# Kernel tuning notes

Measured on AMD Instinct MI355X. Metric: run time of the kernel, lower is better.

## Reference

```python
import jax, jax.numpy as jnp
import numpy as np

HIDDEN = 3584
NUM_HEADS = 28
NUM_KV_HEADS = 4
HEAD_DIM = 128
ROPE_THETA = 1000000.0
B, S = 2, 2048


def setup_inputs() -> dict:
    key = jax.random.key(0)
    k1, k2, k3, k4 = jax.random.split(key, 4)
    q_size = NUM_HEADS * HEAD_DIM
    kv_size = NUM_KV_HEADS * HEAD_DIM
    return {
        "positions": jnp.arange(B * S, dtype=jnp.int32).reshape(B, S),
        "hidden_states": jax.random.normal(k1, (B, S, HIDDEN), dtype=jnp.float32),
        "w_qkv": jax.random.normal(k2, (HIDDEN, q_size + 2 * kv_size), dtype=jnp.float32) * (HIDDEN ** -0.5),
        "b_qkv": jax.random.normal(k3, (q_size + 2 * kv_size,), dtype=jnp.float32) * 0.02,
        "w_o": jax.random.normal(k4, (q_size, HIDDEN), dtype=jnp.float32) * (q_size ** -0.5),
    }


def _rope_cos_sin(positions):
    # NeoX-style rotary embedding, rotary_dim == head_dim
    half = HEAD_DIM // 2
    inv_freq = 1.0 / (ROPE_THETA ** (jnp.arange(0, half, dtype=jnp.float32) * 2.0 / HEAD_DIM))
    angles = positions.astype(jnp.float32)[..., None] * inv_freq  # [B, S, half]
    return jnp.cos(angles), jnp.sin(angles)


def _apply_rope(x, cos, sin):
    # x: [B, S, H, D]; cos/sin: [B, S, half] -> broadcast over heads
    x1, x2 = jnp.split(x, 2, axis=-1)
    c = cos[:, :, None, :]
    s = sin[:, :, None, :]
    return jnp.concatenate([x1 * c - x2 * s, x2 * c + x1 * s], axis=-1)


def reference(positions, hidden_states, w_qkv, b_qkv, w_o):
    q_size = NUM_HEADS * HEAD_DIM
    kv_size = NUM_KV_HEADS * HEAD_DIM
    scaling = HEAD_DIM ** -0.5
    groups = NUM_HEADS // NUM_KV_HEADS

    qkv = hidden_states @ w_qkv + b_qkv  # [B, S, q+2kv]
    q, k, v = jnp.split(qkv, [q_size, q_size + kv_size], axis=-1)
    q = q.reshape(B, S, NUM_HEADS, HEAD_DIM)
    k = k.reshape(B, S, NUM_KV_HEADS, HEAD_DIM)
    v = v.reshape(B, S, NUM_KV_HEADS, HEAD_DIM)

    cos, sin = _rope_cos_sin(positions)
    q = _apply_rope(q, cos, sin)
    k = _apply_rope(k, cos, sin)

    # GQA: group query heads over kv heads. q: [B, S, Hkv, G, D]
    qg = q.reshape(B, S, NUM_KV_HEADS, groups, HEAD_DIM)
    scores = jnp.einsum("bqhgd,bkhd->bhgqk", qg, k) * scaling  # [B, Hkv, G, S, S]
    causal = jnp.tril(jnp.ones((S, S), dtype=bool))
    scores = jnp.where(causal, scores, jnp.finfo(scores.dtype).min)
    probs = jax.nn.softmax(scores, axis=-1)
    o = jnp.einsum("bhgqk,bkhd->bqhgd", probs, v)  # [B, S, Hkv, G, D]
    o = o.reshape(B, S, NUM_HEADS * HEAD_DIM)
    return o @ w_o  # [B, S, HIDDEN]
```

## Files before the change

### kernel.cpp

```cpp
#include <hip/hip_runtime.h>

typedef unsigned short u16;
typedef unsigned int u32;
typedef __bf16 bf16x8 __attribute__((ext_vector_type(8)));
typedef float f32x4 __attribute__((ext_vector_type(4)));

#define NHEAD 28
#define NKVH 4
#define HD 128
#define NB 2
#define NS 2048
#define NTOK 4096
#define HIDDEN_DIM 3584
#define QKVW 4608
#define QSZ 3584
#define KOFF 3584
#define VOFF 4096
#define VSLAB (NTOK * 512)
#define NJOBS 896
#define ATTN_BLOCKS 512
#define QSCALE_L2E 0.12751744f

__device__ __forceinline__ float bf2f(u16 u) {
  u32 x = ((u32)u) << 16; float f; __builtin_memcpy(&f, &x, 4); return f;
}
__device__ __forceinline__ u16 f2bf(float f) {
  u32 x; __builtin_memcpy(&x, &f, 4);
  x += 0x7FFFu + ((x >> 16) & 1u);
  return (u16)(x >> 16);
}
__device__ __forceinline__ u32 pack2bf(float a, float b) {
  __bf16 lo = (__bf16)a, hi = (__bf16)b;
  u16 ul, uh;
  __builtin_memcpy(&ul, &lo, 2); __builtin_memcpy(&uh, &hi, 2);
  return (u32)ul | ((u32)uh << 16);
}
__device__ __forceinline__ void async16(const void* g, void* lds) {
  __builtin_amdgcn_global_load_lds((const __attribute__((address_space(1))) void*)g,
                                   (__attribute__((address_space(3))) void*)lds,
                                   16, 0, 0);
}

#define SB __builtin_amdgcn_sched_barrier(0)
#define BAR do { SB; __builtin_amdgcn_s_barrier(); SB; } while (0)

__global__ void cast_f32_bf16(const float* __restrict__ in, u16* __restrict__ out) {
  int i = (blockIdx.x * 256 + threadIdx.x) * 4;
  float4 v = *(const float4*)(in + i);
  u32 p0 = (u32)f2bf(v.x) | ((u32)f2bf(v.y) << 16);
  u32 p1 = (u32)f2bf(v.z) | ((u32)f2bf(v.w) << 16);
  uint2 r; r.x = p0; r.y = p1;
  *(uint2*)(out + i) = r;
}

__global__ void transpose_cast(const float* __restrict__ in, u16* __restrict__ out,
                               int R, int C) {
  __shared__ float tile[32][33];
  int tx = threadIdx.x & 31, ty = threadIdx.x >> 5;
  int c0 = blockIdx.x * 32, r0 = blockIdx.y * 32;
#pragma unroll
  for (int i = 0; i < 32; i += 8)
    tile[ty + i][tx] = in[(size_t)(r0 + ty + i) * C + c0 + tx];
  __syncthreads();
#pragma unroll
  for (int i = 0; i < 32; i += 8)
    out[(size_t)(c0 + ty + i) * R + r0 + tx] = f2bf(tile[tx][ty + i]);
}

__global__ void rope_table(const int* __restrict__ positions,
                           float* __restrict__ cs, float* __restrict__ sn,
                           int* __restrict__ ctr) {
  if (blockIdx.x == 0 && threadIdx.x == 0) *ctr = 0;
  int idx = blockIdx.x * 256 + threadIdx.x;
  int t = idx >> 6, i = idx & 63;
  float p = (float)positions[t];
  float inv = expf(-(float)i * (13.815510557964274f / 64.f));
  float a = p * inv;
  cs[idx] = cosf(a);
  sn[idx] = sinf(a);
}

__global__ void rope_kernel(u16* __restrict__ qkv, const float* __restrict__ cs,
                            const float* __restrict__ sn) {
  int w = threadIdx.x >> 6, l = threadIdx.x & 63;
  int rid = blockIdx.x * 4 + w;
  int t = rid >> 5, hh = rid & 31;
  size_t base = (size_t)t * QKVW + (hh < NHEAD ? hh * HD : KOFF + (hh - NHEAD) * HD);
  float x1 = bf2f(qkv[base + l]), x2 = bf2f(qkv[base + l + 64]);
  float c = cs[t * 64 + l], s = sn[t * 64 + l];
  float y1 = x1 * c - x2 * s;
  float y2 = x2 * c + x1 * s;
  if (hh < NHEAD) { y1 *= QSCALE_L2E; y2 *= QSCALE_L2E; }
  qkv[base + l] = f2bf(y1);
  qkv[base + l + 64] = f2bf(y2);
}

template <int MODE>
__global__ __launch_bounds__(512, 2) void gemm256(
    const u16* __restrict__ A, const u16* __restrict__ Bt,
    const float* __restrict__ bias, u16* __restrict__ outb,
    float* __restrict__ outf, int M, int Next, int Kst, int ldc, int NT) {
  __shared__ __align__(16) u16 Al[2][256 * 64];
  __shared__ __align__(16) u16 Bl[2][256 * 64];
  const int tid = threadIdx.x;
  const int l = tid & 63, w = tid >> 6;
  const int g = l >> 4, r = l & 15;
  const int wm = w >> 2, wn = w & 3;
  const int nbx = Next >> 8;
  const int cpx = (int)gridDim.x >> 3;
  const int bid = ((int)blockIdx.x & 7) * cpx + ((int)blockIdx.x >> 3);
  int bx, by, kbase;
  float* outp = outf;
  if (MODE == 2) {
    const int tps = nbx * (M >> 8);
    const int ks = bid / tps, rem = bid % tps;
    by = rem / nbx; bx = rem % nbx;
    kbase = ks * (NT << 6);
    outp = outf + (size_t)ks * M * Next;
  } else {
    bx = bid % nbx; by = bid / nbx; kbase = 0;
  }
  const int row0 = by * 256, col0 = bx * 256;

  f32x4 acc[8][4] = {};
  bf16x8 af[4][2];
  bf16x8 bfr[2][2][2];

  auto stageU = [&](const u16* mb, int base0, char* ldsMat, int h, int t) {
#pragma unroll
    for (int q = 0; q < 2; ++q) {
      const int idx = q * 512 + tid;
      const int rho = h * 128 + (idx >> 3);
      const int sl = (idx & 7) ^ (rho & 7);
      async16(mb + (size_t)(base0 + rho) * Kst + kbase + t * 64 + sl * 8,
              ldsMat + (size_t)(t & 1) * 32768 + h * 16384 + idx * 16);
    }
  };

#define READ_A(s, rh)                                                           \
  _Pragma("unroll") for (int fr = 0; fr < 4; ++fr) {                            \
    const int row_ = (rh) * 128 + wm * 64 + fr * 16 + r;                        \
    _Pragma("unroll") for (int kk = 0; kk < 2; ++kk) {                          \
      const int sl_ = (kk * 4 + g) ^ (row_ & 7);                                \
      af[fr][kk] = *(const bf16x8*)((const char*)Al + (s) * 32768 +             \
                                    row_ * 128 + sl_ * 16);                     \
    }                                                                           \
  }
#define READ_B(s, ch)                                                           \
  _Pragma("unroll") for (int fc = 0; fc < 2; ++fc) {                            \
    const int col_ = (ch) * 128 + wn * 32 + fc * 16 + r;                        \
    _Pragma("unroll") for (int kk = 0; kk < 2; ++kk) {                          \
      const int sl_ = (kk * 4 + g) ^ (col_ & 7);                                \
      bfr[ch][fc][kk] = *(const bf16x8*)((const char*)Bl + (s) * 32768 +        \
                                         col_ * 128 + sl_ * 16);                \
    }                                                                           \
  }
#define MFMA_Q(rh, ch)                                                          \
  __builtin_amdgcn_s_setprio(1);                                                \
  _Pragma("unroll") for (int fr = 0; fr < 4; ++fr)                              \
  _Pragma("unroll") for (int fc = 0; fc < 2; ++fc)                              \
  _Pragma("unroll") for (int kk = 0; kk < 2; ++kk)                              \
    acc[(rh) * 4 + fr][(ch) * 2 + fc] = __builtin_amdgcn_mfma_f32_16x16x32_bf16( \
        af[fr][kk], bfr[ch][fc][kk], acc[(rh) * 4 + fr][(ch) * 2 + fc], 0, 0, 0);\
  __builtin_amdgcn_s_setprio(0);

  stageU(A, row0, (char*)Al, 0, 0); stageU(A, row0, (char*)Al, 1, 0);
  stageU(Bt, col0, (char*)Bl, 0, 0); stageU(Bt, col0, (char*)Bl, 1, 0);
  stageU(A, row0, (char*)Al, 0, 1); stageU(Bt, col0, (char*)Bl, 0, 1);
  SB; asm volatile("s_waitcnt vmcnt(4)" ::: "memory");
  BAR;

  for (int t = 0; t < NT; ++t) {
    const int s = t & 1;
    READ_A(s, 0); READ_B(s, 0);
    if (t + 1 < NT) stageU(A, row0, (char*)Al, 1, t + 1);
    BAR; MFMA_Q(0, 0); BAR;
    READ_B(s, 1);
    if (t + 1 < NT) stageU(Bt, col0, (char*)Bl, 1, t + 1);
    BAR; MFMA_Q(0, 1); BAR;
    READ_A(s, 1);
    if (t + 2 < NT) stageU(A, row0, (char*)Al, 0, t + 2);
    BAR; MFMA_Q(1, 0); BAR;
    if (t + 2 < NT) stageU(Bt, col0, (char*)Bl, 0, t + 2);
    BAR; MFMA_Q(1, 1);
    if (t < NT - 2)        { SB; asm volatile("s_waitcnt vmcnt(4)" ::: "memory"); }
    else if (t == NT - 2)  { SB; asm volatile("s_waitcnt vmcnt(0)" ::: "memory"); }
    BAR;
  }
  SB; asm volatile("s_waitcnt vmcnt(0)" ::: "memory");

#pragma unroll
  for (int m = 0; m < 8; ++m) {
    const int row = row0 + (m >> 2) * 128 + wm * 64 + (m & 3) * 16 + g * 4;
#pragma unroll
    for (int n = 0; n < 4; ++n) {
      const int col = col0 + (n >> 1) * 128 + wn * 32 + (n & 1) * 16 + r;
      const float bb = (MODE == 0) ? bias[col] : 0.f;
#pragma unroll
      for (int j = 0; j < 4; ++j) {
        float v = acc[m][n][j] + bb;
        if (MODE == 0) outb[(size_t)(row + j) * ldc + col] = f2bf(v);
        else           outp[(size_t)(row + j) * ldc + col] = v;
      }
    }
  }
}

__global__ void v_reduce(const float* __restrict__ slabs, const float* __restrict__ bias,
                         u16* __restrict__ vtg) {
  __shared__ float tile[32][33];
  const int tx = threadIdx.x & 31, ty = threadIdx.x >> 5;
  const int c0 = blockIdx.x * 32;
  const int r0 = blockIdx.y * 32;
#pragma unroll
  for (int i = 0; i < 32; i += 8) {
    const size_t idx = (size_t)(r0 + ty + i) * 512 + c0 + tx;
    float s = slabs[idx] + slabs[idx + VSLAB] + slabs[idx + 2 * VSLAB] +
              slabs[idx + 3 * VSLAB];
    tile[ty + i][tx] = s + bias[VOFF + c0 + tx];
  }
  __syncthreads();
#pragma unroll
  for (int i = 0; i < 32; i += 8) {
    const int col = c0 + ty + i;
    const int row = r0 + tx;
    vtg[((size_t)((((row >> 11) * NKVH) + (col >> 7)) * HD + (col & 127))) * NS +
        (row & 2047)] = f2bf(tile[tx][ty + i]);
  }
}

__global__ __launch_bounds__(512) void attn_kernel(const u16* __restrict__ qkv,
                                                   const u16* __restrict__ vtg,
                                                   u16* __restrict__ Oh,
                                                   int* __restrict__ ctr) {
  __shared__ __align__(16) u16 Ks[2][64 * 128];
  __shared__ __align__(16) u16 Vt[2][128 * 64];
  __shared__ int s_job;
  const int tid = threadIdx.x, l = tid & 63, w = tid >> 6;
  const int g = l >> 4, r = l & 15;
  const int srcA = r + ((l & 16) << 1);
  const int srcB = srcA + 16;
  const bool hi = (l & 32) != 0;

  for (;;) {
    if (tid == 0) s_job = atomicAdd(ctr, 1);
    __syncthreads();
    const int jid = s_job;
    if (jid >= NJOBS) return;
    const int qtr = jid / 56;
    const int qt = 15 - qtr;
    const int bh = jid - qtr * 56;
    const int h = bh % NHEAD, b = bh / NHEAD;
    const int kvh = h / 7;
    const int q0 = qt * 128;

    const int qrow = q0 + w * 16 + r;
    const size_t qbase = (size_t)(b * NS + qrow) * QKVW + h * HD;
    bf16x8 qf[4];
#pragma unroll
    for (int ks = 0; ks < 4; ++ks)
      qf[ks] = *(const bf16x8*)(qkv + qbase + ks * 32 + g * 8);

    const u16* kb0 = qkv + (size_t)(b * NS) * QKVW + KOFF + kvh * HD;
    const u16* vb0 = vtg + (size_t)((b * NKVH + kvh) * HD) * NS;

    const u16* kap[2];
    const u16* vap[2];
#pragma unroll
    for (int i = 0; i < 2; ++i) {
      const int li = (w * 2 + i) * 64 + l;
      const int rr = li >> 4, c = li & 15;
      kap[i] = kb0 + (size_t)rr * QKVW + ((c ^ (rr & 7)) << 3);
      const int d = li >> 3, c2 = li & 7;
      vap[i] = vb0 + (size_t)d * NS + ((c2 ^ (d & 7)) << 3);
    }

    f32x4 oacc[8] = {};
    float mrun = -1e30f, lsum = 0.f;

    const int nkv = 2 * qt + 2;

    auto stageK = [&](u16* kdst) {
#pragma unroll
      for (int i = 0; i < 2; ++i) {
        async16(kap[i], (char*)kdst + (w * 2 + i) * 1024);
        kap[i] += 64 * QKVW;
      }
    };
    auto stageV = [&](u16* vdst) {
#pragma unroll
      for (int i = 0; i < 2; ++i) {
        async16(vap[i], (char*)vdst + (w * 2 + i) * 1024);
        vap[i] += 64;
      }
    };

    stageK(Ks[0]); stageV(Vt[0]);
    int cur = 0;

    for (int kvt = 0; kvt < nkv; ++kvt) {
      const int kv0 = kvt * 64;
      asm volatile("s_waitcnt vmcnt(2)" ::: "memory");
      __builtin_amdgcn_s_barrier();
      __builtin_amdgcn_sched_barrier(0);

      const bool haveNext = (kvt + 1 < nkv);
      if (haveNext) { stageK(Ks[cur ^ 1]); stageV(Vt[cur ^ 1]); }

      const bool active = kv0 <= q0 + w * 16 + 15;

      union { u32 wrd[4]; bf16x8 v; } pf[2];
      if (active) {
        f32x4 sacc[4] = {};
        const char* ksB = (const char*)Ks[cur];
        __builtin_amdgcn_s_setprio(1);
#pragma unroll
        for (int n = 0; n < 4; ++n) {
          const int key = n * 16 + r;
          const int sw = (key & 7) << 4;
#pragma unroll
          for (int ks = 0; ks < 4; ++ks) {
            bf16x8 kf = *(const bf16x8*)(ksB + key * 256 + ((ks * 64 + g * 16) ^ sw));
            sacc[n] = __builtin_amdgcn_mfma_f32_16x16x32_bf16(kf, qf[ks], sacc[n], 0, 0, 0);
          }
        }
        __builtin_amdgcn_s_setprio(0);
        if (kv0 + 63 > q0 + w * 16) {
#pragma unroll
          for (int n = 0; n < 4; ++n) {
            const int key_g = kv0 + n * 16 + g * 4;
#pragma unroll
            for (int j = 0; j < 4; ++j)
              if (key_g + j > qrow) sacc[n][j] = -1e30f;
          }
        }
        float mx = fmaxf(fmaxf(sacc[0][0], sacc[0][1]), fmaxf(sacc[0][2], sacc[0][3]));
#pragma unroll
        for (int n = 1; n < 4; ++n)
          mx = fmaxf(mx, fmaxf(fmaxf(sacc[n][0], sacc[n][1]), fmaxf(sacc[n][2], sacc[n][3])));
        if (!__all(mx <= mrun + 8.0f)) {
          mx = fmaxf(mx, __shfl_xor(mx, 16, 64));
          mx = fmaxf(mx, __shfl_xor(mx, 32, 64));
          const float mnew = fmaxf(mrun, mx);
          const float scale = __builtin_amdgcn_exp2f(mrun - mnew);
          mrun = mnew;
          lsum *= scale;
#pragma unroll
          for (int dt = 0; dt < 8; ++dt) oacc[dt] *= scale;
        }
#pragma unroll
        for (int n = 0; n < 4; ++n)
#pragma unroll
          for (int j = 0; j < 4; ++j) {
            float p = __builtin_amdgcn_exp2f(sacc[n][j] - mrun);
            sacc[n][j] = p;
            lsum += p;
          }

        u32 pk[4][2];
#pragma unroll
        for (int n = 0; n < 4; ++n) {
          pk[n][0] = pack2bf(sacc[n][0], sacc[n][1]);
          pk[n][1] = pack2bf(sacc[n][2], sacc[n][3]);
        }
#pragma unroll
        for (int ks2 = 0; ks2 < 2; ++ks2) {
          const int n0 = 2 * ks2, n1 = 2 * ks2 + 1;
#pragma unroll
          for (int hh2 = 0; hh2 < 2; ++hh2) {
            u32 a0 = (u32)__shfl((int)pk[n0][hh2], srcA, 64);
            u32 a1 = (u32)__shfl((int)pk[n1][hh2], srcA, 64);
            pf[ks2].wrd[hh2] = hi ? a1 : a0;
            u32 b0 = (u32)__shfl((int)pk[n0][hh2], srcB, 64);
            u32 b1 = (u32)__shfl((int)pk[n1][hh2], srcB, 64);
            pf[ks2].wrd[2 + hh2] = hi ? b1 : b0;
          }
        }
      }

      if (haveNext) asm volatile("s_waitcnt vmcnt(4)" ::: "memory");
      else          asm volatile("s_waitcnt vmcnt(0)" ::: "memory");
      __builtin_amdgcn_s_barrier();
      __builtin_amdgcn_sched_barrier(0);
      if (active) {
        const char* vtB = (const char*)Vt[cur];
        __builtin_amdgcn_s_setprio(1);
#pragma unroll
        for (int ks2 = 0; ks2 < 2; ++ks2) {
#pragma unroll
          for (int dt = 0; dt < 8; ++dt) {
            const int d = dt * 16 + r;
            bf16x8 vf = *(const bf16x8*)(vtB + d * 128 +
                                         ((ks2 * 64 + g * 16) ^ ((d & 7) << 4)));
            oacc[dt] = __builtin_amdgcn_mfma_f32_16x16x32_bf16(vf, pf[ks2].v, oacc[dt], 0, 0, 0);
          }
        }
        __builtin_amdgcn_s_setprio(0);
      }
      cur ^= 1;
    }

    float lr = lsum;
    lr += __shfl_xor(lr, 16, 64);
    lr += __shfl_xor(lr, 32, 64);
    const float inv = 1.f / lr;
    const size_t obase = (size_t)(b * NS + qrow) * QSZ + h * HD;
#pragma unroll
    for (int dt = 0; dt < 8; ++dt) {
      uint2 r2;
      r2.x = pack2bf(oacc[dt][0] * inv, oacc[dt][1] * inv);
      r2.y = pack2bf(oacc[dt][2] * inv, oacc[dt][3] * inv);
      *(uint2*)(Oh + obase + dt * 16 + 4 * g) = r2;
    }
  }
}

extern "C" void kernel_launch(void* const* d_in, const int* in_sizes, int n_in,
                              void* d_out, int out_size, void* d_ws, size_t ws_size,
                              hipStream_t stream) {
  const int* positions = (const int*)d_in[0];
  const float* hidden = (const float*)d_in[1];
  const float* w_qkv = (const float*)d_in[2];
  const float* b_qkv = (const float*)d_in[3];
  const float* w_o = (const float*)d_in[4];
  float* out = (float*)d_out;

  char* ws = (char*)d_ws;
  const size_t XB_OFF = 0;
  const size_t WQT_OFF = 29360128;
  const size_t QKV_OFF = WQT_OFF + 33030144;
  const size_t CS_OFF = QKV_OFF + 37748736;
  const size_t SN_OFF = CS_OFF + 1048576;
  const size_t CTR_OFF = SN_OFF + 1048576;
  const size_t WS_NEED = CTR_OFF + 64;
  if (ws_size < WS_NEED) return;

  u16* Xb = (u16*)(ws + XB_OFF);
  u16* WoT = (u16*)(ws + XB_OFF);
  u16* WqT = (u16*)(ws + WQT_OFF);
  u16* Oh = (u16*)(ws + WQT_OFF);
  u16* qkvb = (u16*)(ws + QKV_OFF);
  float* cs = (float*)(ws + CS_OFF);
  float* sn = (float*)(ws + SN_OFF);
  int* ctr = (int*)(ws + CTR_OFF);
  u16* vtg = (u16*)d_out;
  float* vslabs = (float*)((char*)d_out + 4194304);

  cast_f32_bf16<<<14336, 256, 0, stream>>>(hidden, Xb);
  transpose_cast<<<dim3(QKVW / 32, HIDDEN_DIM / 32), 256, 0, stream>>>(w_qkv, WqT, HIDDEN_DIM, QKVW);
  rope_table<<<(NTOK * 64) / 256, 256, 0, stream>>>(positions, cs, sn, ctr);

  gemm256<0><<<256, 512, 0, stream>>>(
      Xb, WqT, b_qkv, qkvb, nullptr, NTOK, 4096, HIDDEN_DIM, QKVW, HIDDEN_DIM / 64);

  gemm256<2><<<128, 512, 0, stream>>>(
      Xb, WqT + (size_t)VOFF * HIDDEN_DIM, nullptr, nullptr, vslabs,
      NTOK, 512, HIDDEN_DIM, 512, HIDDEN_DIM / 64 / 4);

  v_reduce<<<dim3(512 / 32, NTOK / 32), 256, 0, stream>>>(vslabs, b_qkv, vtg);

  rope_kernel<<<(NTOK * 32) / 4, 256, 0, stream>>>(qkvb, cs, sn);

  transpose_cast<<<dim3(HIDDEN_DIM / 32, QSZ / 32), 256, 0, stream>>>(w_o, WoT, QSZ, HIDDEN_DIM);

  attn_kernel<<<ATTN_BLOCKS, 512, 0, stream>>>(qkvb, vtg, Oh, ctr);

  gemm256<1><<<(HIDDEN_DIM / 256) * (NTOK / 256), 512, 0, stream>>>(
      Oh, WoT, nullptr, nullptr, out, NTOK, HIDDEN_DIM, QSZ, HIDDEN_DIM, QSZ / 64);
}
```

Before: 444.6 us.

## Use 4-wave attention blocks with two query tiles per wave and single-buffered V

Restructures the attention kernel so each of 4 waves handles 32 query rows (two 16-row MFMA tiles), reusing every K and V fragment read from LDS for two MFMAs. This halves LDS reads per MFMA and shrinks the block to 256 threads with a single V buffer, and the grid grows to 768 blocks. In exchange, V is now loaded at the start of each iteration behind a full vmcnt(0) wait instead of being double-buffered, which exposes more load latency. Register pressure also roughly doubles for the accumulators.

```diff
diff --git a/kernel.cpp b/kernel.cpp
--- a/kernel.cpp
+++ b/kernel.cpp
@@ -18,7 +18,7 @@
 #define VOFF 4096
 #define VSLAB (NTOK * 512)
 #define NJOBS 896
-#define ATTN_BLOCKS 512
+#define ATTN_BLOCKS 768
 #define QSCALE_L2E 0.12751744f
 
 __device__ __forceinline__ float bf2f(u16 u) {
@@ -229,12 +229,12 @@
   }
 }
 
-__global__ __launch_bounds__(512) void attn_kernel(const u16* __restrict__ qkv,
+__global__ __launch_bounds__(256) void attn_kernel(const u16* __restrict__ qkv,
                                                    const u16* __restrict__ vtg,
                                                    u16* __restrict__ Oh,
                                                    int* __restrict__ ctr) {
   __shared__ __align__(16) u16 Ks[2][64 * 128];
-  __shared__ __align__(16) u16 Vt[2][128 * 64];
+  __shared__ __align__(16) u16 Vt[128 * 64];
   __shared__ int s_job;
   const int tid = threadIdx.x, l = tid & 63, w = tid >> 6;
   const int g = l >> 4, r = l & 15;
@@ -254,64 +254,69 @@
     const int kvh = h / 7;
     const int q0 = qt * 128;
 
-    const int qrow = q0 + w * 16 + r;
-    const size_t qbase = (size_t)(b * NS + qrow) * QKVW + h * HD;
-    bf16x8 qf[4];
-#pragma unroll
-    for (int ks = 0; ks < 4; ++ks)
-      qf[ks] = *(const bf16x8*)(qkv + qbase + ks * 32 + g * 8);
+    const int qrow0 = q0 + w * 32 + r;
+    const int qrow1 = qrow0 + 16;
+    const size_t qb0 = (size_t)(b * NS + qrow0) * QKVW + h * HD;
+    const size_t qb1 = (size_t)(b * NS + qrow1) * QKVW + h * HD;
+    bf16x8 qf0[4], qf1[4];
+#pragma unroll
+    for (int ks = 0; ks < 4; ++ks) {
+      qf0[ks] = *(const bf16x8*)(qkv + qb0 + ks * 32 + g * 8);
+      qf1[ks] = *(const bf16x8*)(qkv + qb1 + ks * 32 + g * 8);
+    }
 
     const u16* kb0 = qkv + (size_t)(b * NS) * QKVW + KOFF + kvh * HD;
     const u16* vb0 = vtg + (size_t)((b * NKVH + kvh) * HD) * NS;
 
-    const u16* kap[2];
-    const u16* vap[2];
-#pragma unroll
-    for (int i = 0; i < 2; ++i) {
-      const int li = (w * 2 + i) * 64 + l;
+    const u16* kap[4];
+    const u16* vap[4];
+#pragma unroll
+    for (int i = 0; i < 4; ++i) {
+      const int li = (w * 4 + i) * 64 + l;
       const int rr = li >> 4, c = li & 15;
       kap[i] = kb0 + (size_t)rr * QKVW + ((c ^ (rr & 7)) << 3);
       const int d = li >> 3, c2 = li & 7;
       vap[i] = vb0 + (size_t)d * NS + ((c2 ^ (d & 7)) << 3);
     }
 
-    f32x4 oacc[8] = {};
-    float mrun = -1e30f, lsum = 0.f;
+    f32x4 oa0[8] = {}, oa1[8] = {};
+    float m0 = -1e30f, m1 = -1e30f, ls0 = 0.f, ls1 = 0.f;
 
     const int nkv = 2 * qt + 2;
 
     auto stageK = [&](u16* kdst) {
 #pragma unroll
-      for (int i = 0; i < 2; ++i) {
-        async16(kap[i], (char*)kdst + (w * 2 + i) * 1024);
+      for (int i = 0; i < 4; ++i) {
+        async16(kap[i], (char*)kdst + (w * 4 + i) * 1024);
         kap[i] += 64 * QKVW;
       }
     };
-    auto stageV = [&](u16* vdst) {
-#pragma unroll
-      for (int i = 0; i < 2; ++i) {
-        async16(vap[i], (char*)vdst + (w * 2 + i) * 1024);
+    auto stageV = [&]() {
+#pragma unroll
+      for (int i = 0; i < 4; ++i) {
+        async16(vap[i], (char*)Vt + (w * 4 + i) * 1024);
         vap[i] += 64;
       }
     };
 
-    stageK(Ks[0]); stageV(Vt[0]);
+    stageK(Ks[0]);
     int cur = 0;
 
     for (int kvt = 0; kvt < nkv; ++kvt) {
       const int kv0 = kvt * 64;
-      asm volatile("s_waitcnt vmcnt(2)" ::: "memory");
+      asm volatile("s_waitcnt vmcnt(0) lgkmcnt(0)" ::: "memory");
       __builtin_amdgcn_s_barrier();
       __builtin_amdgcn_sched_barrier(0);
 
+      stageV();
       const bool haveNext = (kvt + 1 < nkv);
-      if (haveNext) { stageK(Ks[cur ^ 1]); stageV(Vt[cur ^ 1]); }
-
-      const bool active = kv0 <= q0 + w * 16 + 15;
-
-      union { u32 wrd[4]; bf16x8 v; } pf[2];
+      if (haveNext) stageK(Ks[cur ^ 1]);
+
+      const bool active = kv0 <= q0 + w * 32 + 31;
+
+      union { u32 wrd[4]; bf16x8 v; } pf0[2], pf1[2];
       if (active) {
-        f32x4 sacc[4] = {};
+        f32x4 s0[4] = {}, s1[4] = {};
         const char* ksB = (const char*)Ks[cur];
         __builtin_amdgcn_s_setprio(1);
 #pragma unroll
@@ -321,59 +326,106 @@
 #pragma unroll
           for (int ks = 0; ks < 4; ++ks) {
             bf16x8 kf = *(const bf16x8*)(ksB + key * 256 + ((ks * 64 + g * 16) ^ sw));
-            sacc[n] = __builtin_amdgcn_mfma_f32_16x16x32_bf16(kf, qf[ks], sacc[n], 0, 0, 0);
+            s0[n] = __builtin_amdgcn_mfma_f32_16x16x32_bf16(kf, qf0[ks], s0[n], 0, 0, 0);
+            s1[n] = __builtin_amdgcn_mfma_f32_16x16x32_bf16(kf, qf1[ks], s1[n], 0, 0, 0);
           }
         }
         __builtin_amdgcn_s_setprio(0);
-        if (kv0 + 63 > q0 + w * 16) {
+        if (kv0 + 63 > q0 + w * 32) {
 #pragma unroll
           for (int n = 0; n < 4; ++n) {
             const int key_g = kv0 + n * 16 + g * 4;
 #pragma unroll
-            for (int j = 0; j < 4; ++j)
-              if (key_g + j > qrow) sacc[n][j] = -1e30f;
+            for (int j = 0; j < 4; ++j) {
+              if (key_g + j > qrow0) s0[n][j] = -1e30f;
+              if (key_g + j > qrow1) s1[n][j] = -1e30f;
+            }
           }
         }
-        float mx = fmaxf(fmaxf(sacc[0][0], sacc[0][1]), fmaxf(sacc[0][2], sacc[0][3]));
-#pragma unroll
-        for (int n = 1; n < 4; ++n)
-          mx = fmaxf(mx, fmaxf(fmaxf(sacc[n][0], sacc[n][1]), fmaxf(sacc[n][2], sacc[n][3])));
-        if (!__all(mx <= mrun + 8.0f)) {
-          mx = fmaxf(mx, __shfl_xor(mx, 16, 64));
-          mx = fmaxf(mx, __shfl_xor(mx, 32, 64));
-          const float mnew = fmaxf(mrun, mx);
-          const float scale = __builtin_amdgcn_exp2f(mrun - mnew);
-          mrun = mnew;
-          lsum *= scale;
-#pragma unroll
-          for (int dt = 0; dt < 8; ++dt) oacc[dt] *= scale;
+        {
+          float mx = fmaxf(fmaxf(s0[0][0], s0[0][1]), fmaxf(s0[0][2], s0[0][3]));
+#pragma unroll
+          for (int n = 1; n < 4; ++n)
+            mx = fmaxf(mx, fmaxf(fmaxf(s0[n][0], s0[n][1]), fmaxf(s0[n][2], s0[n][3])));
+          if (!__all(mx <= m0 + 8.0f)) {
+            mx = fmaxf(mx, __shfl_xor(mx, 16, 64));
+            mx = fmaxf(mx, __shfl_xor(mx, 32, 64));
+            const float mnew = fmaxf(m0, mx);
+            const float scale = __builtin_amdgcn_exp2f(m0 - mnew);
+            m0 = mnew;
+            ls0 *= scale;
+#pragma unroll
+            for (int dt = 0; dt < 8; ++dt) oa0[dt] *= scale;
+          }
+#pragma unroll
+          for (int n = 0; n < 4; ++n)
+#pragma unroll
+            for (int j = 0; j < 4; ++j) {
+              float p = __builtin_amdgcn_exp2f(s0[n][j] - m0);
+              s0[n][j] = p;
+              ls0 += p;
+            }
+          u32 pk[4][2];
+#pragma unroll
+          for (int n = 0; n < 4; ++n) {
+            pk[n][0] = pack2bf(s0[n][0], s0[n][1]);
+            pk[n][1] = pack2bf(s0[n][2], s0[n][3]);
+          }
+#pragma unroll
+          for (int ks2 = 0; ks2 < 2; ++ks2) {
+            const int n0 = 2 * ks2, n1 = 2 * ks2 + 1;
+#pragma unroll
+            for (int hh2 = 0; hh2 < 2; ++hh2) {
+              u32 a0 = (u32)__shfl((int)pk[n0][hh2], srcA, 64);
+              u32 a1 = (u32)__shfl((int)pk[n1][hh2], srcA, 64);
+              pf0[ks2].wrd[hh2] = hi ? a1 : a0;
+              u32 b0 = (u32)__shfl((int)pk[n0][hh2], srcB, 64);
+              u32 b1 = (u32)__shfl((int)pk[n1][hh2], srcB, 64);
+              pf0[ks2].wrd[2 + hh2] = hi ? b1 : b0;
+            }
+          }
         }
-#pragma unroll
-        for (int n = 0; n < 4; ++n)
-#pragma unroll
-          for (int j = 0; j < 4; ++j) {
-            float p = __builtin_amdgcn_exp2f(sacc[n][j] - mrun);
-            sacc[n][j] = p;
-            lsum += p;
-          }
-
-        u32 pk[4][2];
-#pragma unroll
-        for (int n = 0; n < 4; ++n) {
-          pk[n][0] = pack2bf(sacc[n][0], sacc[n][1]);
-          pk[n][1] = pack2bf(sacc[n][2], sacc[n][3]);
-        }
-#pragma unroll
-        for (int ks2 = 0; ks2 < 2; ++ks2) {
-          const int n0 = 2 * ks2, n1 = 2 * ks2 + 1;
-#pragma unroll
-          for (int hh2 = 0; hh2 < 2; ++hh2) {
-            u32 a0 = (u32)__shfl((int)pk[n0][hh2], srcA, 64);
-            u32 a1 = (u32)__shfl((int)pk[n1][hh2], srcA, 64);
-            pf[ks2].wrd[hh2] = hi ? a1 : a0;
-            u32 b0 = (u32)__shfl((int)pk[n0][hh2], srcB, 64);
-            u32 b1 = (u32)__shfl((int)pk[n1][hh2], srcB, 64);
-            pf[ks2].wrd[2 + hh2] = hi ? b1 : b0;
+        {
+          float mx = fmaxf(fmaxf(s1[0][0], s1[0][1]), fmaxf(s1[0][2], s1[0][3]));
+#pragma unroll
+          for (int n = 1; n < 4; ++n)
+            mx = fmaxf(mx, fmaxf(fmaxf(s1[n][0], s1[n][1]), fmaxf(s1[n][2], s1[n][3])));
+          if (!__all(mx <= m1 + 8.0f)) {
+            mx = fmaxf(mx, __shfl_xor(mx, 16, 64));
+            mx = fmaxf(mx, __shfl_xor(mx, 32, 64));
+            const float mnew = fmaxf(m1, mx);
+            const float scale = __builtin_amdgcn_exp2f(m1 - mnew);
+            m1 = mnew;
+            ls1 *= scale;
+#pragma unroll
+            for (int dt = 0; dt < 8; ++dt) oa1[dt] *= scale;
+          }
+#pragma unroll
+          for (int n = 0; n < 4; ++n)
+#pragma unroll
+            for (int j = 0; j < 4; ++j) {
+              float p = __builtin_amdgcn_exp2f(s1[n][j] - m1);
+              s1[n][j] = p;
+              ls1 += p;
+            }
+          u32 pk[4][2];
+#pragma unroll
+          for (int n = 0; n < 4; ++n) {
+            pk[n][0] = pack2bf(s1[n][0], s1[n][1]);
+            pk[n][1] = pack2bf(s1[n][2], s1[n][3]);
+          }
+#pragma unroll
+          for (int ks2 = 0; ks2 < 2; ++ks2) {
+            const int n0 = 2 * ks2, n1 = 2 * ks2 + 1;
+#pragma unroll
+            for (int hh2 = 0; hh2 < 2; ++hh2) {
+              u32 a0 = (u32)__shfl((int)pk[n0][hh2], srcA, 64);
+              u32 a1 = (u32)__shfl((int)pk[n1][hh2], srcA, 64);
+              pf1[ks2].wrd[hh2] = hi ? a1 : a0;
+              u32 b0 = (u32)__shfl((int)pk[n0][hh2], srcB, 64);
+              u32 b1 = (u32)__shfl((int)pk[n1][hh2], srcB, 64);
+              pf1[ks2].wrd[2 + hh2] = hi ? b1 : b0;
+            }
           }
         }
       }
@@ -383,7 +435,7 @@
       __builtin_amdgcn_s_barrier();
       __builtin_amdgcn_sched_barrier(0);
       if (active) {
-        const char* vtB = (const char*)Vt[cur];
+        const char* vtB = (const char*)Vt;
         __builtin_amdgcn_s_setprio(1);
 #pragma unroll
         for (int ks2 = 0; ks2 < 2; ++ks2) {
@@ -392,7 +444,8 @@
             const int d = dt * 16 + r;
             bf16x8 vf = *(const bf16x8*)(vtB + d * 128 +
                                          ((ks2 * 64 + g * 16) ^ ((d & 7) << 4)));
-            oacc[dt] = __builtin_amdgcn_mfma_f32_16x16x32_bf16(vf, pf[ks2].v, oacc[dt], 0, 0, 0);
+            oa0[dt] = __builtin_amdgcn_mfma_f32_16x16x32_bf16(vf, pf0[ks2].v, oa0[dt], 0, 0, 0);
+            oa1[dt] = __builtin_amdgcn_mfma_f32_16x16x32_bf16(vf, pf1[ks2].v, oa1[dt], 0, 0, 0);
           }
         }
         __builtin_amdgcn_s_setprio(0);
@@ -400,17 +453,33 @@
       cur ^= 1;
     }
 
-    float lr = lsum;
-    lr += __shfl_xor(lr, 16, 64);
-    lr += __shfl_xor(lr, 32, 64);
-    const float inv = 1.f / lr;
-    const size_t obase = (size_t)(b * NS + qrow) * QSZ + h * HD;
-#pragma unroll
-    for (int dt = 0; dt < 8; ++dt) {
-      uint2 r2;
-      r2.x = pack2bf(oacc[dt][0] * inv, oacc[dt][1] * inv);
-      r2.y = pack2bf(oacc[dt][2] * inv, oacc[dt][3] * inv);
-      *(uint2*)(Oh + obase + dt * 16 + 4 * g) = r2;
+    {
+      float lr = ls0;
+      lr += __shfl_xor(lr, 16, 64);
+      lr += __shfl_xor(lr, 32, 64);
+      const float inv = 1.f / lr;
+      const size_t obase = (size_t)(b * NS + qrow0) * QSZ + h * HD;
+#pragma unroll
+      for (int dt = 0; dt < 8; ++dt) {
+        uint2 r2;
+        r2.x = pack2bf(oa0[dt][0] * inv, oa0[dt][1] * inv);
+        r2.y = pack2bf(oa0[dt][2] * inv, oa0[dt][3] * inv);
+        *(uint2*)(Oh + obase + dt * 16 + 4 * g) = r2;
+      }
+    }
+    {
+      float lr = ls1;
+      lr += __shfl_xor(lr, 16, 64);
+      lr += __shfl_xor(lr, 32, 64);
+      const float inv = 1.f / lr;
+      const size_t obase = (size_t)(b * NS + qrow1) * QSZ + h * HD;
+#pragma unroll
+      for (int dt = 0; dt < 8; ++dt) {
+        uint2 r2;
+        r2.x = pack2bf(oa1[dt][0] * inv, oa1[dt][1] * inv);
+        r2.y = pack2bf(oa1[dt][2] * inv, oa1[dt][3] * inv);
+        *(uint2*)(Oh + obase + dt * 16 + 4 * g) = r2;
+      }
     }
   }
 }
@@ -463,7 +532,7 @@
 
   transpose_cast<<<dim3(HIDDEN_DIM / 32, QSZ / 32), 256, 0, stream>>>(w_o, WoT, QSZ, HIDDEN_DIM);
 
-  attn_kernel<<<ATTN_BLOCKS, 512, 0, stream>>>(qkvb, vtg, Oh, ctr);
+  attn_kernel<<<ATTN_BLOCKS, 256, 0, stream>>>(qkvb, vtg, Oh, ctr);
 
   gemm256<1><<<(HIDDEN_DIM / 256) * (NTOK / 256), 512, 0, stream>>>(
       Oh, WoT, nullptr, nullptr, out, NTOK, HIDDEN_DIM, QSZ, HIDDEN_DIM, QSZ / 64);
```

After: 473.1 us. +6.4%, slower.
